# Kernel optimization log

Measured on AMD Instinct MI355X. Metric: run time of the kernel, lower is better.

Reference implementation:

```python
import jax, jax.numpy as jnp
import numpy as np

N0, N1, N2, N3 = 524288, 262144, 65536, 8192
E0, E1, E2 = 2621440, 655360, 81920
D_IN, D_H, D_OUT = 256, 256, 64


def setup_inputs() -> dict:
    key = jax.random.key(0)
    ks = jax.random.split(key, 16)
    s = 0.02
    inp = {
        "x": jax.random.normal(ks[0], (N0, D_IN), dtype=jnp.float32),
        "src0": jax.random.randint(ks[1], (E0,), 0, N0, dtype=jnp.int32),
        "dst0": jax.random.randint(ks[2], (E0,), 0, N1, dtype=jnp.int32),
        "src1": jax.random.randint(ks[3], (E1,), 0, N1, dtype=jnp.int32),
        "dst1": jax.random.randint(ks[4], (E1,), 0, N2, dtype=jnp.int32),
        "src2": jax.random.randint(ks[5], (E2,), 0, N2, dtype=jnp.int32),
        "dst2": jax.random.randint(ks[6], (E2,), 0, N3, dtype=jnp.int32),
        "nd0": N1, "nd1": N2, "nd2": N3,
        "Wfc": jax.random.normal(ks[7], (D_IN, D_H), dtype=jnp.float32) * s,
        "bfc": jnp.zeros((D_H,), dtype=jnp.float32),
        "Ws0": jax.random.normal(ks[8], (D_H, D_H), dtype=jnp.float32) * s,
        "Wn0": jax.random.normal(ks[9], (D_H, D_H), dtype=jnp.float32) * s,
        "b0": jnp.zeros((D_H,), dtype=jnp.float32),
        "Ws1": jax.random.normal(ks[10], (D_H, D_H), dtype=jnp.float32) * s,
        "Wn1": jax.random.normal(ks[11], (D_H, D_H), dtype=jnp.float32) * s,
        "b1": jnp.zeros((D_H,), dtype=jnp.float32),
        "Ws2": jax.random.normal(ks[12], (D_H, D_OUT), dtype=jnp.float32) * s,
        "Wn2": jax.random.normal(ks[13], (D_H, D_OUT), dtype=jnp.float32) * s,
        "b2": jnp.zeros((D_OUT,), dtype=jnp.float32),
    }
    return inp


def sage_conv(h, src, dst, n_dst, Ws, Wn, b):
    # DGL SAGEConv 'mean': out = h_dst @ W_self + mean_neigh(h_src) @ W_neigh + b
    h_dst = h[:n_dst]
    msg = jnp.take(h, src, axis=0)                    # [E, d] gather
    agg = jax.ops.segment_sum(msg, dst, num_segments=n_dst)
    cnt = jax.ops.segment_sum(jnp.ones((dst.shape[0],), h.dtype), dst, num_segments=n_dst)
    mean = agg / jnp.maximum(cnt, 1.0)[:, None]
    return h_dst @ Ws + mean @ Wn + b


def reference(x, src0, dst0, src1, dst1, src2, dst2, nd0, nd1, nd2,
              Wfc, bfc, Ws0, Wn0, b0, Ws1, Wn1, b1, Ws2, Wn2, b2):
    h = jax.nn.relu(x @ Wfc + bfc)                    # input projection (dropout=0 -> identity)
    h = jax.nn.relu(sage_conv(h, src0, dst0, nd0, Ws0, Wn0, b0))
    h = jax.nn.relu(sage_conv(h, src1, dst1, nd1, Ws1, Wn1, b1))
    h = sage_conv(h, src2, dst2, nd2, Ws2, Wn2, b2)   # no activation on final layer
    return h
```

## Files before the change

### kernel.cpp

```cpp
#include <hip/hip_runtime.h>

constexpr int N0c = 524288, N1c = 262144, N2c = 65536, N3c = 8192;
constexpr int NTOT = N1c + N2c + N3c;

typedef __attribute__((ext_vector_type(8))) short   bf16x8;
typedef __attribute__((ext_vector_type(4))) float   f32x4;
typedef __attribute__((ext_vector_type(8))) unsigned short u16x8;

__device__ inline unsigned short f2bf(float f) {
    union { float f; unsigned u; } v; v.f = f;
    unsigned r = v.u + 0x7FFF + ((v.u >> 16) & 1);
    return (unsigned short)(r >> 16);
}
__device__ inline float bf2f(unsigned short u) {
    union { unsigned u; float f; } v; v.u = ((unsigned)u) << 16;
    return v.f;
}

__device__ inline void glds16(const void* g, void* l) {
    __builtin_amdgcn_global_load_lds(
        (const __attribute__((address_space(1))) unsigned int*)g,
        (__attribute__((address_space(3))) unsigned int*)l, 16, 0, 0);
}

struct WPack { const float* w[7]; unsigned short* o[7]; };

__global__ __launch_bounds__(256)
void wconv_all(WPack p, int* __restrict__ hist)
{
    if (blockIdx.x >= 1408) {
        const int zid = (blockIdx.x - 1408) * 256 + threadIdx.x;
        ((int4*)hist)[zid] = make_int4(0, 0, 0, 0);
        return;
    }
    const int idx = blockIdx.x * 256 + threadIdx.x;
    int widx, off, N;
    if (idx < 327680) { widx = idx >> 16; off = idx & 65535; N = 256; }
    else {
        const int r = idx - 327680;
        widx = 5 + (r >> 14); off = r & 16383; N = 64;
        if (widx > 6) return;
    }
    const int k = off / N, n = off % N;
    p.o[widx][n * 256 + k] = f2bf(p.w[widx][off]);
}

__device__ inline bf16x8 pack_bf8(const float* p) {
    const f32x4 u = *(const f32x4*)p;
    const f32x4 v = *(const f32x4*)(p + 4);
    bf16x8 t;
    #pragma unroll
    for (int j = 0; j < 4; ++j) {
        t[j]     = (short)f2bf(u[j]);
        t[j + 4] = (short)f2bf(v[j]);
    }
    return t;
}

struct CsrArgs {
    const int* src0; const int* dst0;
    const int* src1; const int* dst1;
    const int* src2; const int* dst2;
    int e0, e01, etot;
};

template<int KC>
__device__ inline const unsigned short*
frag_src(const unsigned short* Wt, int r, int kh)
{
    constexpr int SK = KC / 32;
    const int s  = r >> 6;
    const int l  = r & 63;
    const int nt = s / SK;
    const int k0i = s % SK;
    const int n  = nt * 16 + (l & 15);
    const int kg = k0i * 4 + (l >> 4);
    return Wt + n * 256 + kh * KC + kg * 8;
}

__global__ __launch_bounds__(512, 2)
void fc_rank_k(const float* __restrict__ A1f, const unsigned short* __restrict__ Wt1,
               const float* __restrict__ bias, unsigned short* __restrict__ Cv,
               CsrArgs a, int* __restrict__ hist, int* __restrict__ rank,
               int gemmBlocks)
{
    if ((int)blockIdx.x >= gemmBlocks) {
        const int i = ((int)blockIdx.x - gemmBlocks) * 512 + (int)threadIdx.x;
        if (i >= a.etot) return;
        const int* dstp; int e, hb;
        if (i < a.e0)       { dstp = a.dst0; e = i;         hb = 0; }
        else if (i < a.e01) { dstp = a.dst1; e = i - a.e0;  hb = N1c; }
        else                { dstp = a.dst2; e = i - a.e01; hb = N1c + N2c; }
        rank[i] = atomicAdd(&hist[hb + dstp[e]], 1);
        return;
    }

    constexpr int KC = 128, SK = KC / 32;
    __shared__ unsigned short Bs[4096 * 8];

    const int t    = threadIdx.x;
    const int lane = t & 63;
    const int wv   = t >> 6;
    const int col  = lane & 15;
    const int kg   = lane >> 4;
    const long row0 = (long)blockIdx.x * 128 + wv * 16;

    f32x4 acc[16];
    #pragma unroll
    for (int nt = 0; nt < 16; ++nt) acc[nt] = (f32x4){0.f, 0.f, 0.f, 0.f};

    const long ar = (row0 + col) * 256;

    for (int kh = 0; kh < 2; ++kh) {
        if (kh) __syncthreads();
        #pragma unroll
        for (int it = 0; it < 8; ++it) {
            const int g = it * 512 + t;
            glds16(frag_src<KC>(Wt1, g, kh), &Bs[(it * 512 + wv * 64) * 8]);
        }
        __syncthreads();

        #pragma unroll
        for (int k0i = 0; k0i < SK; ++k0i) {
            const bf16x8 a1 = pack_bf8(&A1f[ar + kh * KC + k0i * 32 + kg * 8]);
            #pragma unroll
            for (int nt = 0; nt < 16; ++nt) {
                const bf16x8 b1 = *(const bf16x8*)&Bs[((nt * SK + k0i) * 64 + lane) * 8];
                acc[nt] = __builtin_amdgcn_mfma_f32_16x16x32_bf16(a1, b1, acc[nt], 0, 0, 0);
            }
        }
    }

    #pragma unroll
    for (int nt = 0; nt < 16; ++nt) {
        const int c = nt * 16 + col;
        const float bb = bias[c];
        #pragma unroll
        for (int rr = 0; rr < 4; ++rr) {
            const long row = row0 + kg * 4 + rr;
            Cv[row * 256 + c] = f2bf(fmaxf(acc[nt][rr] + bb, 0.f));
        }
    }
}

template<int NT, int KC, bool DUAL, bool RELU, bool A_F32, bool OUT_BF16>
__global__ __launch_bounds__(512, 2)
void gemm2(const void* __restrict__ A1v, const void* __restrict__ A2v,
           const unsigned short* __restrict__ Wt1,
           const unsigned short* __restrict__ Wt2,
           const float* __restrict__ bias, void* __restrict__ Cv)
{
    constexpr int N     = NT * 16;
    constexpr int PH    = 256 / KC;
    constexpr int SK    = KC / 32;
    constexpr int GPM   = 64 * NT * SK;
    constexpr int TOTG  = GPM * (DUAL ? 2 : 1);
    static_assert(TOTG == 4096, "LDS sizing");
    __shared__ unsigned short Bs[TOTG * 8];

    const int t    = threadIdx.x;
    const int lane = t & 63;
    const int wv   = t >> 6;
    const int col  = lane & 15;
    const int kg   = lane >> 4;
    const long row0 = (long)blockIdx.x * 128 + wv * 16;

    const unsigned short* A1h = (const unsigned short*)A1v;
    const float*          A1f = (const float*)A1v;
    const unsigned short* A2h = (const unsigned short*)A2v;

    f32x4 acc[NT];
    #pragma unroll
    for (int nt = 0; nt < NT; ++nt) acc[nt] = (f32x4){0.f, 0.f, 0.f, 0.f};

    const long ar = (row0 + col) * 256;

    for (int kh = 0; kh < PH; ++kh) {
        if (kh) __syncthreads();
        #pragma unroll
        for (int it = 0; it < TOTG / 512; ++it) {
            const int g = it * 512 + t;
            const int m = DUAL ? (g / GPM) : 0;
            const int r = DUAL ? (g % GPM) : g;
            glds16(frag_src<KC>(m ? Wt2 : Wt1, r, kh),
                   &Bs[(it * 512 + wv * 64) * 8]);
        }
        __syncthreads();

        #pragma unroll
        for (int k0i = 0; k0i < SK; ++k0i) {
            const long ac = ar + kh * KC + k0i * 32 + kg * 8;
            bf16x8 a1, a2;
            if constexpr (A_F32) a1 = pack_bf8(&A1f[ac]);
            else                 a1 = *(const bf16x8*)&A1h[ac];
            if constexpr (DUAL)  a2 = *(const bf16x8*)&A2h[ac];
            #pragma unroll
            for (int nt = 0; nt < NT; ++nt) {
                const bf16x8 b1 = *(const bf16x8*)&Bs[((nt * SK + k0i) * 64 + lane) * 8];
                acc[nt] = __builtin_amdgcn_mfma_f32_16x16x32_bf16(a1, b1, acc[nt], 0, 0, 0);
                if constexpr (DUAL) {
                    const bf16x8 b2 = *(const bf16x8*)&Bs[(GPM + (nt * SK + k0i) * 64 + lane) * 8];
                    acc[nt] = __builtin_amdgcn_mfma_f32_16x16x32_bf16(a2, b2, acc[nt], 0, 0, 0);
                }
            }
        }
    }

    #pragma unroll
    for (int nt = 0; nt < NT; ++nt) {
        const int c = nt * 16 + col;
        const float bb = bias[c];
        #pragma unroll
        for (int rr = 0; rr < 4; ++rr) {
            const long row = row0 + kg * 4 + rr;
            float o = acc[nt][rr] + bb;
            if constexpr (RELU) o = fmaxf(o, 0.f);
            if constexpr (OUT_BF16)
                ((unsigned short*)Cv)[row * N + c] = f2bf(o);
            else
                ((float*)Cv)[row * N + c] = o;
        }
    }
}

__global__ __launch_bounds__(256)
void scan1_k(const int* __restrict__ hist, int* __restrict__ offs,
             int* __restrict__ bsum, int n)
{
    __shared__ int sm[256];
    const int t = threadIdx.x;
    const int base = blockIdx.x * 1024 + t * 4;
    int4 v = make_int4(0, 0, 0, 0);
    if (base < n) v = *(const int4*)&hist[base];
    const int s = v.x + v.y + v.z + v.w;
    int val = s;
    sm[t] = val; __syncthreads();
    #pragma unroll
    for (int off = 1; off < 256; off <<= 1) {
        const int add = (t >= off) ? sm[t - off] : 0;
        __syncthreads();
        val += add;
        sm[t] = val;
        __syncthreads();
    }
    const int excl = val - s;
    if (base < n) {
        offs[base]     = excl;
        offs[base + 1] = excl + v.x;
        offs[base + 2] = excl + v.x + v.y;
        offs[base + 3] = excl + v.x + v.y + v.z;
    }
    if (t == 255) bsum[blockIdx.x] = val;
}

__global__ __launch_bounds__(512)
void scan2_k(int* __restrict__ bsum, int nb)
{
    __shared__ int sm[512];
    const int t = threadIdx.x;
    const int s = (t < nb) ? bsum[t] : 0;
    int val = s;
    sm[t] = val; __syncthreads();
    #pragma unroll
    for (int off = 1; off < 512; off <<= 1) {
        const int add = (t >= off) ? sm[t - off] : 0;
        __syncthreads();
        val += add;
        sm[t] = val;
        __syncthreads();
    }
    if (t < nb) bsum[t] = val - s;
}

__global__ __launch_bounds__(256)
void scan3_k(int* __restrict__ offs, const int* __restrict__ bsum, int etot)
{
    const int i = blockIdx.x * 256 + threadIdx.x;
    offs[i] += bsum[i >> 10];
    if (i == 0) offs[NTOT] = etot;
}

__global__ __launch_bounds__(256)
void place_k(CsrArgs a, const int* __restrict__ offs, const int* __restrict__ rank,
             int* __restrict__ ssrc)
{
    const int i = blockIdx.x * 256 + threadIdx.x;
    if (i >= a.etot) return;
    const int* dstp; const int* srcp; int e, hb;
    if (i < a.e0)       { dstp = a.dst0; srcp = a.src0; e = i;         hb = 0; }
    else if (i < a.e01) { dstp = a.dst1; srcp = a.src1; e = i - a.e0;  hb = N1c; }
    else                { dstp = a.dst2; srcp = a.src2; e = i - a.e01; hb = N1c + N2c; }
    const int g = hb + dstp[e];
    ssrc[offs[g] + rank[i]] = srcp[e];
}

__global__ __launch_bounds__(256)
void agg_k(const unsigned short* __restrict__ h, const int* __restrict__ ssrc,
           const int* __restrict__ ob, unsigned short* __restrict__ agg, int n)
{
    const int w    = blockIdx.x * 4 + (threadIdx.x >> 6);
    const int lane = threadIdx.x & 63;
    if (w >= n) return;
    const int beg = ob[w];
    const int end = ob[w + 1];
    const int hf  = lane >> 5;
    const int co  = (lane & 31) * 8;

    float acc[8] = {0.f, 0.f, 0.f, 0.f, 0.f, 0.f, 0.f, 0.f};

    int j = beg;
    for (; j + 16 <= end; j += 16) {
        u16x8 v[8];
        #pragma unroll
        for (int q = 0; q < 8; ++q)
            v[q] = *(const u16x8*)&h[(size_t)ssrc[j + 2 * q + hf] * 256 + co];
        #pragma unroll
        for (int q = 0; q < 8; ++q)
            #pragma unroll
            for (int c = 0; c < 8; ++c) acc[c] += bf2f(v[q][c]);
    }
    const int rem = end - j;
    if (rem > 8) {
        u16x8 v[8]; bool ok[8];
        #pragma unroll
        for (int q = 0; q < 8; ++q) {
            const int e = j + 2 * q + hf;
            ok[q] = (e < end);
            v[q] = *(const u16x8*)&h[(size_t)ssrc[ok[q] ? e : (end - 1)] * 256 + co];
        }
        #pragma unroll
        for (int q = 0; q < 8; ++q)
            #pragma unroll
            for (int c = 0; c < 8; ++c) acc[c] += ok[q] ? bf2f(v[q][c]) : 0.0f;
    } else if (rem > 0) {
        u16x8 v[4]; bool ok[4];
        #pragma unroll
        for (int q = 0; q < 4; ++q) {
            const int e = j + 2 * q + hf;
            ok[q] = (e < end);
            v[q] = *(const u16x8*)&h[(size_t)ssrc[ok[q] ? e : (end - 1)] * 256 + co];
        }
        #pragma unroll
        for (int q = 0; q < 4; ++q)
            #pragma unroll
            for (int c = 0; c < 8; ++c) acc[c] += ok[q] ? bf2f(v[q][c]) : 0.0f;
    }

    #pragma unroll
    for (int c = 0; c < 8; ++c) acc[c] += __shfl_xor(acc[c], 32);

    if (hf == 0) {
        const float inv = 1.0f / fmaxf((float)(end - beg), 1.0f);
        u16x8 o;
        #pragma unroll
        for (int c = 0; c < 8; ++c) o[c] = f2bf(acc[c] * inv);
        *(u16x8*)&agg[(size_t)w * 256 + co] = o;
    }
}

extern "C" void kernel_launch(void* const* d_in, const int* in_sizes, int n_in,
                              void* d_out, int out_size, void* d_ws, size_t ws_size,
                              hipStream_t stream)
{
    const float* x    = (const float*)d_in[0];
    const int*   src0 = (const int*)d_in[1];
    const int*   dst0 = (const int*)d_in[2];
    const int*   src1 = (const int*)d_in[3];
    const int*   dst1 = (const int*)d_in[4];
    const int*   src2 = (const int*)d_in[5];
    const int*   dst2 = (const int*)d_in[6];
    const float* Wfc  = (const float*)d_in[10];
    const float* bfc  = (const float*)d_in[11];
    const float* Ws0  = (const float*)d_in[12];
    const float* Wn0  = (const float*)d_in[13];
    const float* b0   = (const float*)d_in[14];
    const float* Ws1  = (const float*)d_in[15];
    const float* Wn1  = (const float*)d_in[16];
    const float* b1   = (const float*)d_in[17];
    const float* Ws2  = (const float*)d_in[18];
    const float* Wn2  = (const float*)d_in[19];
    const float* b2   = (const float*)d_in[20];
    const int E0 = in_sizes[1], E1 = in_sizes[3], E2 = in_sizes[5];
    const int Etot = E0 + E1 + E2;

    char* ws = (char*)d_ws;
    unsigned short* h0   = (unsigned short*)ws;
    unsigned short* h1   = (unsigned short*)(ws + (256ULL << 20));
    unsigned short* h2   = (unsigned short*)(ws + (384ULL << 20));
    unsigned short* agg  = (unsigned short*)(ws + (416ULL << 20));
    unsigned short* Wt   = (unsigned short*)(ws + (544ULL << 20));
    int*            hist = (int*)(ws + (545ULL << 20));
    int*            offs = (int*)(ws + (547ULL << 20));
    int*            bsum = (int*)(ws + (549ULL << 20));
    int*            ssrc = (int*)(ws + (550ULL << 20));
    int*            rank = (int*)(ws + (564ULL << 20));

    unsigned short* wfc = Wt;
    unsigned short* ws0 = Wt + 65536;
    unsigned short* wn0 = Wt + 131072;
    unsigned short* ws1 = Wt + 196608;
    unsigned short* wn1 = Wt + 262144;
    unsigned short* ws2 = Wt + 327680;
    unsigned short* wn2 = Wt + 344064;

    const dim3 blk(256);

    WPack wp;
    wp.w[0] = Wfc; wp.w[1] = Ws0; wp.w[2] = Wn0; wp.w[3] = Ws1; wp.w[4] = Wn1;
    wp.w[5] = Ws2; wp.w[6] = Wn2;
    wp.o[0] = wfc; wp.o[1] = ws0; wp.o[2] = wn0; wp.o[3] = ws1; wp.o[4] = wn1;
    wp.o[5] = ws2; wp.o[6] = wn2;
    wconv_all<<<dim3(1408 + 328), blk, 0, stream>>>(wp, hist);

    CsrArgs ca;
    ca.src0 = src0; ca.dst0 = dst0; ca.src1 = src1; ca.dst1 = dst1;
    ca.src2 = src2; ca.dst2 = dst2;
    ca.e0 = E0; ca.e01 = E0 + E1; ca.etot = Etot;
    const int gemmBlocks = N0c / 128;
    const int rankBlocks = (Etot + 511) / 512;
    fc_rank_k<<<dim3(gemmBlocks + rankBlocks), dim3(512), 0, stream>>>(
        x, wfc, bfc, h0, ca, hist, rank, gemmBlocks);

    scan1_k<<<dim3(NTOT / 1024), blk, 0, stream>>>(hist, offs, bsum, NTOT);
    scan2_k<<<dim3(1), dim3(512), 0, stream>>>(bsum, NTOT / 1024);
    scan3_k<<<dim3(NTOT / 256), blk, 0, stream>>>(offs, bsum, Etot);
    place_k<<<dim3((Etot + 255) / 256), blk, 0, stream>>>(ca, offs, rank, ssrc);

    agg_k<<<dim3(N1c / 4), blk, 0, stream>>>(h0, ssrc, offs, agg, N1c);
    gemm2<16, 64, true, true, false, true><<<dim3(N1c / 128), dim3(512), 0, stream>>>(
        h0, agg, ws0, wn0, b0, h1);

    agg_k<<<dim3(N2c / 4), blk, 0, stream>>>(h1, ssrc, offs + N1c, agg, N2c);
    gemm2<16, 64, true, true, false, true><<<dim3(N2c / 128), dim3(512), 0, stream>>>(
        h1, agg, ws1, wn1, b1, h2);

    agg_k<<<dim3(N3c / 4), blk, 0, stream>>>(h2, ssrc, offs + N1c + N2c, agg, N3c);
    gemm2<4, 256, true, false, false, false><<<dim3(N3c / 128), dim3(512), 0, stream>>>(
        h2, agg, ws2, wn2, b2, (float*)d_out);
}
```

Baseline: 922.5 us.

## Double GEMM block tile to 256 rows with 1024-thread blocks and larger K chunks

Pulls the GEMM into one shared device body and launches every GEMM with 1024-thread blocks covering 256 rows. Each weight tile staged in LDS is therefore reused across twice as many rows. The K chunk grows: the input projection loads all of K at once, and the dual GEMMs use 128-wide chunks, so there are fewer barrier phases. In exchange, LDS per block doubles and the launch bounds tighten the per-thread register budget, which may cut residency or cause spills.

```diff
diff --git a/kernel.cpp b/kernel.cpp
--- a/kernel.cpp
+++ b/kernel.cpp
@@ -78,92 +78,25 @@
     return Wt + n * 256 + kh * KC + kg * 8;
 }
 
-__global__ __launch_bounds__(512, 2)
-void fc_rank_k(const float* __restrict__ A1f, const unsigned short* __restrict__ Wt1,
-               const float* __restrict__ bias, unsigned short* __restrict__ Cv,
-               CsrArgs a, int* __restrict__ hist, int* __restrict__ rank,
-               int gemmBlocks)
-{
-    if ((int)blockIdx.x >= gemmBlocks) {
-        const int i = ((int)blockIdx.x - gemmBlocks) * 512 + (int)threadIdx.x;
-        if (i >= a.etot) return;
-        const int* dstp; int e, hb;
-        if (i < a.e0)       { dstp = a.dst0; e = i;         hb = 0; }
-        else if (i < a.e01) { dstp = a.dst1; e = i - a.e0;  hb = N1c; }
-        else                { dstp = a.dst2; e = i - a.e01; hb = N1c + N2c; }
-        rank[i] = atomicAdd(&hist[hb + dstp[e]], 1);
-        return;
-    }
-
-    constexpr int KC = 128, SK = KC / 32;
-    __shared__ unsigned short Bs[4096 * 8];
-
-    const int t    = threadIdx.x;
+template<int NT, int KC, bool DUAL, bool RELU, bool A_F32, bool OUT_BF16>
+__device__ inline void gemm_body(const void* A1v, const void* A2v,
+                                 const unsigned short* Wt1,
+                                 const unsigned short* Wt2,
+                                 const float* bias, void* Cv,
+                                 unsigned short* Bs, int bid, int t)
+{
+    constexpr int N    = NT * 16;
+    constexpr int PH   = 256 / KC;
+    constexpr int SK   = KC / 32;
+    constexpr int GPM  = 64 * NT * SK;
+    constexpr int TOTG = GPM * (DUAL ? 2 : 1);
+    static_assert(TOTG % 1024 == 0, "stage sizing");
+
     const int lane = t & 63;
     const int wv   = t >> 6;
     const int col  = lane & 15;
-    const int kg   = lane >> 4;
-    const long row0 = (long)blockIdx.x * 128 + wv * 16;
-
-    f32x4 acc[16];
-    #pragma unroll
-    for (int nt = 0; nt < 16; ++nt) acc[nt] = (f32x4){0.f, 0.f, 0.f, 0.f};
-
-    const long ar = (row0 + col) * 256;
-
-    for (int kh = 0; kh < 2; ++kh) {
-        if (kh) __syncthreads();
-        #pragma unroll
-        for (int it = 0; it < 8; ++it) {
-            const int g = it * 512 + t;
-            glds16(frag_src<KC>(Wt1, g, kh), &Bs[(it * 512 + wv * 64) * 8]);
-        }
-        __syncthreads();
-
-        #pragma unroll
-        for (int k0i = 0; k0i < SK; ++k0i) {
-            const bf16x8 a1 = pack_bf8(&A1f[ar + kh * KC + k0i * 32 + kg * 8]);
-            #pragma unroll
-            for (int nt = 0; nt < 16; ++nt) {
-                const bf16x8 b1 = *(const bf16x8*)&Bs[((nt * SK + k0i) * 64 + lane) * 8];
-                acc[nt] = __builtin_amdgcn_mfma_f32_16x16x32_bf16(a1, b1, acc[nt], 0, 0, 0);
-            }
-        }
-    }
-
-    #pragma unroll
-    for (int nt = 0; nt < 16; ++nt) {
-        const int c = nt * 16 + col;
-        const float bb = bias[c];
-        #pragma unroll
-        for (int rr = 0; rr < 4; ++rr) {
-            const long row = row0 + kg * 4 + rr;
-            Cv[row * 256 + c] = f2bf(fmaxf(acc[nt][rr] + bb, 0.f));
-        }
-    }
-}
-
-template<int NT, int KC, bool DUAL, bool RELU, bool A_F32, bool OUT_BF16>
-__global__ __launch_bounds__(512, 2)
-void gemm2(const void* __restrict__ A1v, const void* __restrict__ A2v,
-           const unsigned short* __restrict__ Wt1,
-           const unsigned short* __restrict__ Wt2,
-           const float* __restrict__ bias, void* __restrict__ Cv)
-{
-    constexpr int N     = NT * 16;
-    constexpr int PH    = 256 / KC;
-    constexpr int SK    = KC / 32;
-    constexpr int GPM   = 64 * NT * SK;
-    constexpr int TOTG  = GPM * (DUAL ? 2 : 1);
-    static_assert(TOTG == 4096, "LDS sizing");
-    __shared__ unsigned short Bs[TOTG * 8];
-
-    const int t    = threadIdx.x;
-    const int lane = t & 63;
-    const int wv   = t >> 6;
-    const int col  = lane & 15;
-    const int kg   = lane >> 4;
-    const long row0 = (long)blockIdx.x * 128 + wv * 16;
+    const int kq   = lane >> 4;
+    const long row0 = (long)bid * 256 + wv * 16;
 
     const unsigned short* A1h = (const unsigned short*)A1v;
     const float*          A1f = (const float*)A1v;
@@ -175,21 +108,22 @@
 
     const long ar = (row0 + col) * 256;
 
+    #pragma unroll
     for (int kh = 0; kh < PH; ++kh) {
         if (kh) __syncthreads();
         #pragma unroll
-        for (int it = 0; it < TOTG / 512; ++it) {
-            const int g = it * 512 + t;
+        for (int it = 0; it < TOTG / 1024; ++it) {
+            const int g = it * 1024 + t;
             const int m = DUAL ? (g / GPM) : 0;
             const int r = DUAL ? (g % GPM) : g;
             glds16(frag_src<KC>(m ? Wt2 : Wt1, r, kh),
-                   &Bs[(it * 512 + wv * 64) * 8]);
+                   &Bs[(it * 1024 + wv * 64) * 8]);
         }
         __syncthreads();
 
         #pragma unroll
         for (int k0i = 0; k0i < SK; ++k0i) {
-            const long ac = ar + kh * KC + k0i * 32 + kg * 8;
+            const long ac = ar + kh * KC + k0i * 32 + kq * 8;
             bf16x8 a1, a2;
             if constexpr (A_F32) a1 = pack_bf8(&A1f[ac]);
             else                 a1 = *(const bf16x8*)&A1h[ac];
@@ -212,7 +146,7 @@
         const float bb = bias[c];
         #pragma unroll
         for (int rr = 0; rr < 4; ++rr) {
-            const long row = row0 + kg * 4 + rr;
+            const long row = row0 + kq * 4 + rr;
             float o = acc[nt][rr] + bb;
             if constexpr (RELU) o = fmaxf(o, 0.f);
             if constexpr (OUT_BF16)
@@ -221,6 +155,50 @@
                 ((float*)Cv)[row * N + c] = o;
         }
     }
+}
+
+__global__ __launch_bounds__(1024, 4)
+void fc_rank_k(const float* __restrict__ A1f, const unsigned short* __restrict__ Wt1,
+               const float* __restrict__ bias, unsigned short* __restrict__ Cv,
+               CsrArgs a, int* __restrict__ hist, int* __restrict__ rank,
+               int gemmBlocks)
+{
+    __shared__ unsigned short Bs[8192 * 8];
+    if ((int)blockIdx.x >= gemmBlocks) {
+        const int i = ((int)blockIdx.x - gemmBlocks) * 1024 + (int)threadIdx.x;
+        if (i >= a.etot) return;
+        const int* dstp; int e, hb;
+        if (i < a.e0)       { dstp = a.dst0; e = i;         hb = 0; }
+        else if (i < a.e01) { dstp = a.dst1; e = i - a.e0;  hb = N1c; }
+        else                { dstp = a.dst2; e = i - a.e01; hb = N1c + N2c; }
+        rank[i] = atomicAdd(&hist[hb + dstp[e]], 1);
+        return;
+    }
+    gemm_body<16, 256, false, true, true, true>(
+        A1f, nullptr, Wt1, nullptr, bias, Cv, Bs, (int)blockIdx.x, (int)threadIdx.x);
+}
+
+template<bool RELU, bool OUT_BF16>
+__global__ __launch_bounds__(1024, 4)
+void gemm_dual_k(const void* __restrict__ A1v, const void* __restrict__ A2v,
+                 const unsigned short* __restrict__ Wt1,
+                 const unsigned short* __restrict__ Wt2,
+                 const float* __restrict__ bias, void* __restrict__ Cv)
+{
+    __shared__ unsigned short Bs[8192 * 8];
+    gemm_body<16, 128, true, RELU, false, OUT_BF16>(
+        A1v, A2v, Wt1, Wt2, bias, Cv, Bs, (int)blockIdx.x, (int)threadIdx.x);
+}
+
+__global__ __launch_bounds__(1024, 4)
+void gemm_fin_k(const void* __restrict__ A1v, const void* __restrict__ A2v,
+                const unsigned short* __restrict__ Wt1,
+                const unsigned short* __restrict__ Wt2,
+                const float* __restrict__ bias, void* __restrict__ Cv)
+{
+    __shared__ unsigned short Bs[4096 * 8];
+    gemm_body<4, 256, true, false, false, false>(
+        A1v, A2v, Wt1, Wt2, bias, Cv, Bs, (int)blockIdx.x, (int)threadIdx.x);
 }
 
 __global__ __launch_bounds__(256)
@@ -416,9 +394,9 @@
     ca.src0 = src0; ca.dst0 = dst0; ca.src1 = src1; ca.dst1 = dst1;
     ca.src2 = src2; ca.dst2 = dst2;
     ca.e0 = E0; ca.e01 = E0 + E1; ca.etot = Etot;
-    const int gemmBlocks = N0c / 128;
-    const int rankBlocks = (Etot + 511) / 512;
-    fc_rank_k<<<dim3(gemmBlocks + rankBlocks), dim3(512), 0, stream>>>(
+    const int gemmBlocks = N0c / 256;
+    const int rankBlocks = (Etot + 1023) / 1024;
+    fc_rank_k<<<dim3(gemmBlocks + rankBlocks), dim3(1024), 0, stream>>>(
         x, wfc, bfc, h0, ca, hist, rank, gemmBlocks);
 
     scan1_k<<<dim3(NTOT / 1024), blk, 0, stream>>>(hist, offs, bsum, NTOT);
@@ -427,14 +405,14 @@
     place_k<<<dim3((Etot + 255) / 256), blk, 0, stream>>>(ca, offs, rank, ssrc);
 
     agg_k<<<dim3(N1c / 4), blk, 0, stream>>>(h0, ssrc, offs, agg, N1c);
-    gemm2<16, 64, true, true, false, true><<<dim3(N1c / 128), dim3(512), 0, stream>>>(
+    gemm_dual_k<true, true><<<dim3(N1c / 256), dim3(1024), 0, stream>>>(
         h0, agg, ws0, wn0, b0, h1);
 
     agg_k<<<dim3(N2c / 4), blk, 0, stream>>>(h1, ssrc, offs + N1c, agg, N2c);
-    gemm2<16, 64, true, true, false, true><<<dim3(N2c / 128), dim3(512), 0, stream>>>(
+    gemm_dual_k<true, true><<<dim3(N2c / 256), dim3(1024), 0, stream>>>(
         h1, agg, ws1, wn1, b1, h2);
 
     agg_k<<<dim3(N3c / 4), blk, 0, stream>>>(h2, ssrc, offs + N1c + N2c, agg, N3c);
-    gemm2<4, 256, true, false, false, false><<<dim3(N3c / 128), dim3(512), 0, stream>>>(
+    gemm_fin_k<<<dim3(N3c / 256), dim3(1024), 0, stream>>>(
         h2, agg, ws2, wn2, b2, (float*)d_out);
 }
```

Result: faster. 870.3 us (-5.7%).
